# Optimization experiments

Measured on AMD Instinct MI355X. Metric: run time of the kernel, lower is better.

The kernel has to match this reference:

```python
import jax, jax.numpy as jnp
import numpy as np

N_NODES = 100000
N_EDGES = 600000
IN_SIZE = 128
OUT_SIZE = 128
N_GRAPHS = 100
BN_EPS = 1e-5


def setup_inputs() -> dict:
    key = jax.random.key(0)
    ks = jax.random.split(key, 8)
    h = jax.random.normal(ks[0], (N_NODES, IN_SIZE), dtype=jnp.float32)
    norm = jax.random.uniform(ks[1], (N_NODES, 1), dtype=jnp.float32)
    src = jax.random.randint(ks[2], (N_EDGES,), 0, N_NODES, dtype=jnp.int32)
    dst = jax.random.randint(ks[3], (N_EDGES,), 0, N_NODES, dtype=jnp.int32)
    graph_ids = jnp.sort(jax.random.randint(ks[4], (N_NODES,), 0, N_GRAPHS, dtype=jnp.int32))
    # Linear + BatchNorm params
    W = jax.random.normal(ks[5], (IN_SIZE, OUT_SIZE), dtype=jnp.float32) / np.sqrt(IN_SIZE)
    b = jnp.zeros((OUT_SIZE,), dtype=jnp.float32)
    gamma = jnp.ones((OUT_SIZE,), dtype=jnp.float32)
    beta = jnp.zeros((OUT_SIZE,), dtype=jnp.float32)
    return {"h": h, "norm": norm, "W": W, "b": b, "gamma": gamma, "beta": beta,
            "src": src, "dst": dst, "graph_ids": graph_ids}


def reference(h, norm, W, b, gamma, beta, src, dst, graph_ids):
    # pre-normalize, scatter-sum over edges (copy_src + sum), post-normalize
    x = h * norm                                            # [N, in]
    agg = jax.ops.segment_sum(x[src], dst, num_segments=N_NODES)  # SpMM
    x = agg * norm
    # linear + relu
    x = jax.nn.relu(jnp.dot(x, W) + b)                      # [N, out]
    # BatchNorm1d (training-mode: batch mean, biased variance)
    mean = jnp.mean(x, axis=0)
    var = jnp.mean(jnp.square(x - mean), axis=0)
    x = (x - mean) * jax.lax.rsqrt(var + BN_EPS) * gamma + beta
    # sum_nodes pooling per graph
    phis = jax.ops.segment_sum(x, graph_ids, num_segments=N_GRAPHS)  # [G, out]
    return (x, phis)
```

## Files before the change

kernel.cpp:

```cpp
#include <hip/hip_runtime.h>
#include <hip/hip_bf16.h>

#define N_NODES 100000
#define N_PAD 100096
#define N_EDGES 600000
#define CH 128
#define N_GRAPHS 100
#define BN_EPS 1e-5f
#define NBUCKET 32
#define CAP 16
#define OVFCAP 8192
#define EDGE_BLOCKS 2344
#define GEMM_BLOCKS 782
#define GATHER_BLOCKS 2048
#define BN_BLOCKS 1563
#define ZERO_INTS (N_NODES + 2 * NBUCKET * CH + 4)
#define ZERO_BLOCKS 423
#define PHIS_BLOCKS 50
#define WT_BLOCKS 64
#define PRESCALE_BLOCKS 6250

typedef __bf16 bf16x8 __attribute__((ext_vector_type(8)));
typedef float f32x4 __attribute__((ext_vector_type(4)));

__device__ __forceinline__ ushort f2bf(float f) {
    union { float f; unsigned u; } x; x.f = f;
    unsigned u = x.u;
    unsigned r = (u + 0x7fffu + ((u >> 16) & 1u)) >> 16;
    return (ushort)r;
}
__device__ __forceinline__ float bflo(unsigned p) { return __builtin_bit_cast(float, p << 16); }
__device__ __forceinline__ float bfhi(unsigned p) { return __builtin_bit_cast(float, p & 0xffff0000u); }

__global__ __launch_bounds__(256) void k_prep(const float* __restrict__ W,
        const float* __restrict__ h, const float* __restrict__ norm,
        int* __restrict__ zbase, ushort* __restrict__ Wt,
        float* __restrict__ phis, ushort* __restrict__ xh) {
    unsigned bid = blockIdx.x;
    int tid = threadIdx.x;
    if (bid < ZERO_BLOCKS) {
        int i = bid * 256 + tid;
        if (i < ZERO_INTS) zbase[i] = 0;
    } else if (bid < ZERO_BLOCKS + PHIS_BLOCKS) {
        int i = (bid - ZERO_BLOCKS) * 256 + tid;
        phis[i] = 0.f;
    } else if (bid < ZERO_BLOCKS + PHIS_BLOCKS + WT_BLOCKS) {
        int t = (bid - ZERO_BLOCKS - PHIS_BLOCKS) * 256 + tid;
        int k = t >> 7, o = t & 127;
        Wt[o * CH + k] = f2bf(W[t]);
    } else {
        int t = (bid - ZERO_BLOCKS - PHIS_BLOCKS - WT_BLOCKS) * 256 + tid;
        int n = t >> 4, c = (t & 15) << 3;
        float nm = norm[n];
        float4 a = *(const float4*)(h + (size_t)n * CH + c);
        float4 d = *(const float4*)(h + (size_t)n * CH + c + 4);
        uint4 o;
        o.x = (unsigned)f2bf(a.x * nm) | ((unsigned)f2bf(a.y * nm) << 16);
        o.y = (unsigned)f2bf(a.z * nm) | ((unsigned)f2bf(a.w * nm) << 16);
        o.z = (unsigned)f2bf(d.x * nm) | ((unsigned)f2bf(d.y * nm) << 16);
        o.w = (unsigned)f2bf(d.z * nm) | ((unsigned)f2bf(d.w * nm) << 16);
        *(uint4*)(xh + (size_t)n * CH + c) = o;
    }
}

__global__ __launch_bounds__(256) void k_fill(const int* __restrict__ src,
        const int* __restrict__ dst, int* __restrict__ cnt,
        int* __restrict__ ovfcur, int* __restrict__ ovf, int* __restrict__ esrc) {
    int e = blockIdx.x * 256 + threadIdx.x;
    if (e < N_EDGES) {
        int d = dst[e], s = src[e];
        int slot = atomicAdd(&cnt[d], 1);
        if (slot < CAP) __builtin_nontemporal_store(s, &esrc[d * CAP + slot]);
        else { int p = atomicAdd(ovfcur, 1); if (p < OVFCAP) { ovf[2*p] = d; ovf[2*p+1] = s; } }
    }
}

__global__ __launch_bounds__(256) void k_gather(const ushort* __restrict__ xh,
        const float* __restrict__ norm, const int* __restrict__ cnt,
        const int* __restrict__ esrc, const int* __restrict__ ovfcur,
        const int* __restrict__ ovf, ushort* __restrict__ x2) {
    int tid = threadIdx.x;
    int cg = tid & 15, rl = tid >> 4;
    int c = cg * 8;
    int no = min(*ovfcur, OVFCAP);

    for (int n = blockIdx.x * 16 + rl; n < N_PAD; n += GATHER_BLOCKS * 16) {
        if (n >= N_NODES) {
            uint4 z = {0u, 0u, 0u, 0u};
            *(uint4*)(x2 + (size_t)n * CH + c) = z;
            continue;
        }
        int craw = cnt[n];
        int e = min(craw, CAP);
        float nn = norm[n];
        int base = n * CAP;
        float a0=0.f,a1=0.f,a2=0.f,a3=0.f,a4=0.f,a5=0.f,a6=0.f,a7=0.f;
        int j = 0;
        for (; j + 4 <= e; j += 4) {
            int4 s4 = *(const int4*)(esrc + base + j);
            uint4 v0 = *(const uint4*)(xh + (size_t)s4.x * CH + c);
            uint4 v1 = *(const uint4*)(xh + (size_t)s4.y * CH + c);
            uint4 v2 = *(const uint4*)(xh + (size_t)s4.z * CH + c);
            uint4 v3 = *(const uint4*)(xh + (size_t)s4.w * CH + c);
            a0 += bflo(v0.x) + bflo(v1.x) + bflo(v2.x) + bflo(v3.x);
            a1 += bfhi(v0.x) + bfhi(v1.x) + bfhi(v2.x) + bfhi(v3.x);
            a2 += bflo(v0.y) + bflo(v1.y) + bflo(v2.y) + bflo(v3.y);
            a3 += bfhi(v0.y) + bfhi(v1.y) + bfhi(v2.y) + bfhi(v3.y);
            a4 += bflo(v0.z) + bflo(v1.z) + bflo(v2.z) + bflo(v3.z);
            a5 += bfhi(v0.z) + bfhi(v1.z) + bfhi(v2.z) + bfhi(v3.z);
            a6 += bflo(v0.w) + bflo(v1.w) + bflo(v2.w) + bflo(v3.w);
            a7 += bfhi(v0.w) + bfhi(v1.w) + bfhi(v2.w) + bfhi(v3.w);
        }
        for (; j < e; j++) {
            int s = esrc[base + j];
            uint4 v = *(const uint4*)(xh + (size_t)s * CH + c);
            a0 += bflo(v.x); a1 += bfhi(v.x);
            a2 += bflo(v.y); a3 += bfhi(v.y);
            a4 += bflo(v.z); a5 += bfhi(v.z);
            a6 += bflo(v.w); a7 += bfhi(v.w);
        }
        if (craw > CAP && no > 0) {
            for (int i = 0; i < no; i++) {
                if (ovf[2*i] == n) {
                    int s = ovf[2*i+1];
                    uint4 v = *(const uint4*)(xh + (size_t)s * CH + c);
                    a0 += bflo(v.x); a1 += bfhi(v.x);
                    a2 += bflo(v.y); a3 += bfhi(v.y);
                    a4 += bflo(v.z); a5 += bfhi(v.z);
                    a6 += bflo(v.w); a7 += bfhi(v.w);
                }
            }
        }
        uint4 o;
        o.x = (unsigned)f2bf(a0 * nn) | ((unsigned)f2bf(a1 * nn) << 16);
        o.y = (unsigned)f2bf(a2 * nn) | ((unsigned)f2bf(a3 * nn) << 16);
        o.z = (unsigned)f2bf(a4 * nn) | ((unsigned)f2bf(a5 * nn) << 16);
        o.w = (unsigned)f2bf(a6 * nn) | ((unsigned)f2bf(a7 * nn) << 16);
        *(uint4*)(x2 + (size_t)n * CH + c) = o;
    }
}

__global__ __launch_bounds__(256) void k_gemm(const ushort* __restrict__ x2,
        const ushort* __restrict__ Wt, const float* __restrict__ bias,
        ushort* __restrict__ y16, float* __restrict__ psum, float* __restrict__ psq) {
    __shared__ ushort ys[128 * CH];

    int tid = threadIdx.x;
    int w = tid >> 6, L = tid & 63;
    int c15 = L & 15, quad = L >> 4;
    size_t nb = (size_t)blockIdx.x * 128 + w * 32;

    const bf16x8* A0 = (const bf16x8*)(x2 + (nb + c15) * CH);
    const bf16x8* A1 = (const bf16x8*)(x2 + (nb + 16 + c15) * CH);

    f32x4 acc0[8] = {}, acc1[8] = {};
    #pragma unroll
    for (int kt = 0; kt < 4; kt++) {
        bf16x8 a0 = A0[kt * 4 + quad];
        bf16x8 a1 = A1[kt * 4 + quad];
        #pragma unroll
        for (int ot = 0; ot < 8; ot++) {
            bf16x8 b = *(const bf16x8*)(Wt + (size_t)(ot * 16 + c15) * CH + kt * 32 + quad * 8);
            acc0[ot] = __builtin_amdgcn_mfma_f32_16x16x32_bf16(a0, b, acc0[ot], 0, 0, 0);
            acc1[ot] = __builtin_amdgcn_mfma_f32_16x16x32_bf16(a1, b, acc1[ot], 0, 0, 0);
        }
    }

    float sA[8], qA[8];
    #pragma unroll
    for (int ot = 0; ot < 8; ot++) {
        int col = ot * 16 + c15;
        float bv = bias[col];
        float s_ = 0.f, q_ = 0.f;
        #pragma unroll
        for (int r = 0; r < 4; r++) {
            size_t n = nb + quad * 4 + r;
            float v = fmaxf(acc0[ot][r] + bv, 0.f);
            ys[(w * 32 + quad * 4 + r) * CH + col] = f2bf(v);
            if (n < N_NODES) { s_ += v; q_ += v * v; }
            size_t n2 = n + 16;
            float v2 = fmaxf(acc1[ot][r] + bv, 0.f);
            ys[(w * 32 + 16 + quad * 4 + r) * CH + col] = f2bf(v2);
            if (n2 < N_NODES) { s_ += v2; q_ += v2 * v2; }
        }
        sA[ot] = s_; qA[ot] = q_;
    }
    __syncthreads();

    {
        const uint4* ysv = (const uint4*)ys;
        uint4* out = (uint4*)(y16 + (size_t)blockIdx.x * 128 * CH);
        #pragma unroll
        for (int i = 0; i < 8; i++) out[tid + i * 256] = ysv[tid + i * 256];
    }
    __syncthreads();

    float* red = (float*)ys;
    #pragma unroll
    for (int ot = 0; ot < 8; ot++) {
        red[ot * 256 + tid] = sA[ot];
        red[2048 + ot * 256 + tid] = qA[ot];
    }
    __syncthreads();

    if (tid < 128) {
        int ot = tid >> 4, cc = tid & 15;
        int col = ot * 16 + cc;
        float S = 0.f, Q = 0.f;
        #pragma unroll
        for (int g = 0; g < 16; g++) {
            int sl = (g >> 2) * 64 + (g & 3) * 16 + cc;
            S += red[ot * 256 + sl];
            Q += red[2048 + ot * 256 + sl];
        }
        int bucket = blockIdx.x & (NBUCKET - 1);
        atomicAdd(&psum[bucket * CH + col], S);
        atomicAdd(&psq[bucket * CH + col], Q);
    }
}

__global__ void k_finalize(const float* __restrict__ psum, const float* __restrict__ psq,
        const float* __restrict__ gamma, const float* __restrict__ beta,
        float* __restrict__ scale, float* __restrict__ shift) {
    int t = threadIdx.x;
    float S = 0.f, Q = 0.f;
    #pragma unroll
    for (int g = 0; g < NBUCKET; g++) { S += psum[g * CH + t]; Q += psq[g * CH + t]; }
    const float invN = 1.f / (float)N_NODES;
    float mean = S * invN;
    float var  = Q * invN - mean * mean;
    float sc   = gamma[t] * rsqrtf(var + BN_EPS);
    scale[t] = sc;
    shift[t] = beta[t] - mean * sc;
}

__global__ __launch_bounds__(256) void k_bnpool(const ushort* __restrict__ y16,
        const int* __restrict__ gids, const float* __restrict__ scale,
        const float* __restrict__ shift, float* __restrict__ xout,
        float* __restrict__ phis) {
    __shared__ float smP[16][CH];

    int tid = threadIdx.x;
    int cg = tid & 15, rl = tid >> 4;
    int c = cg * 8;
    int r0 = blockIdx.x * 64;
    int rbase = r0 + rl * 4;

    float4 sc0 = *(const float4*)(scale + c), sc1 = *(const float4*)(scale + c + 4);
    float4 sh0 = *(const float4*)(shift + c), sh1 = *(const float4*)(shift + c + 4);

    bool fast = (r0 + 63 < N_NODES) && (gids[r0] == gids[r0 + 63]);

    if (fast) {
        float4 p0 = make_float4(0.f,0.f,0.f,0.f), p1 = make_float4(0.f,0.f,0.f,0.f);
        #pragma unroll
        for (int j = 0; j < 4; j++) {
            int r = rbase + j;
            uint4 v = *(const uint4*)(y16 + (size_t)r * CH + c);
            float4 f0, f1;
            f0.x = fmaf(bflo(v.x), sc0.x, sh0.x); f0.y = fmaf(bfhi(v.x), sc0.y, sh0.y);
            f0.z = fmaf(bflo(v.y), sc0.z, sh0.z); f0.w = fmaf(bfhi(v.y), sc0.w, sh0.w);
            f1.x = fmaf(bflo(v.z), sc1.x, sh1.x); f1.y = fmaf(bfhi(v.z), sc1.y, sh1.y);
            f1.z = fmaf(bflo(v.w), sc1.z, sh1.z); f1.w = fmaf(bfhi(v.w), sc1.w, sh1.w);
            *(float4*)(xout + (size_t)r * CH + c) = f0;
            *(float4*)(xout + (size_t)r * CH + c + 4) = f1;
            p0.x += f0.x; p0.y += f0.y; p0.z += f0.z; p0.w += f0.w;
            p1.x += f1.x; p1.y += f1.y; p1.z += f1.z; p1.w += f1.w;
        }
        *(float4*)&smP[rl][c] = p0;
        *(float4*)&smP[rl][c + 4] = p1;
        __syncthreads();
        if (tid < 128) {
            int g = gids[r0];
            float S = 0.f;
            #pragma unroll
            for (int k = 0; k < 16; k++) S += smP[k][tid];
            atomicAdd(&phis[(size_t)g * CH + tid], S);
        }
    } else {
        float p[8] = {};
        int gprev = -1;
        #pragma unroll
        for (int j = 0; j < 4; j++) {
            int r = rbase + j;
            if (r >= N_NODES) break;
            int g = gids[r];
            if (g != gprev) {
                if (gprev >= 0) {
                    #pragma unroll
                    for (int k = 0; k < 8; k++) {
                        atomicAdd(&phis[(size_t)gprev * CH + c + k], p[k]);
                        p[k] = 0.f;
                    }
                }
                gprev = g;
            }
            uint4 v = *(const uint4*)(y16 + (size_t)r * CH + c);
            float f[8];
            f[0] = fmaf(bflo(v.x), sc0.x, sh0.x); f[1] = fmaf(bfhi(v.x), sc0.y, sh0.y);
            f[2] = fmaf(bflo(v.y), sc0.z, sh0.z); f[3] = fmaf(bfhi(v.y), sc0.w, sh0.w);
            f[4] = fmaf(bflo(v.z), sc1.x, sh1.x); f[5] = fmaf(bfhi(v.z), sc1.y, sh1.y);
            f[6] = fmaf(bflo(v.w), sc1.z, sh1.z); f[7] = fmaf(bfhi(v.w), sc1.w, sh1.w);
            *(float4*)(xout + (size_t)r * CH + c) = make_float4(f[0], f[1], f[2], f[3]);
            *(float4*)(xout + (size_t)r * CH + c + 4) = make_float4(f[4], f[5], f[6], f[7]);
            #pragma unroll
            for (int k = 0; k < 8; k++) p[k] += f[k];
        }
        if (gprev >= 0) {
            #pragma unroll
            for (int k = 0; k < 8; k++)
                atomicAdd(&phis[(size_t)gprev * CH + c + k], p[k]);
        }
    }
}

extern "C" void kernel_launch(void* const* d_in, const int* in_sizes, int n_in,
                              void* d_out, int out_size, void* d_ws, size_t ws_size,
                              hipStream_t stream)
{
    const float* h     = (const float*)d_in[0];
    const float* norm  = (const float*)d_in[1];
    const float* W     = (const float*)d_in[2];
    const float* b     = (const float*)d_in[3];
    const float* gamma = (const float*)d_in[4];
    const float* beta  = (const float*)d_in[5];
    const int*   src   = (const int*)d_in[6];
    const int*   dst   = (const int*)d_in[7];
    const int*   gids  = (const int*)d_in[8];

    float* x_out = (float*)d_out;
    float* phis  = x_out + (size_t)N_NODES * CH;

    ushort* xh   = (ushort*)d_ws;
    ushort* x2   = xh + (size_t)N_NODES * CH;
    ushort* y16  = x2 + (size_t)N_PAD * CH;
    ushort* Wt   = y16 + (size_t)N_PAD * CH;
    int*   cnt     = (int*)(Wt + CH * CH);
    float* psum    = (float*)(cnt + N_NODES);
    float* psq     = psum + NBUCKET * CH;
    int*   ovfcur  = (int*)(psq + NBUCKET * CH);
    int*   esrc    = ovfcur + 4;
    int*   ovf     = esrc + (size_t)N_NODES * CAP;
    float* scale   = (float*)(ovf + 2 * OVFCAP);
    float* shift   = scale + CH;

    k_prep<<<ZERO_BLOCKS + PHIS_BLOCKS + WT_BLOCKS + PRESCALE_BLOCKS, 256, 0, stream>>>(
        W, h, norm, cnt, Wt, phis, xh);
    k_fill<<<EDGE_BLOCKS, 256, 0, stream>>>(src, dst, cnt, ovfcur, ovf, esrc);
    k_gather<<<GATHER_BLOCKS, 256, 0, stream>>>(
        xh, norm, cnt, esrc, ovfcur, ovf, x2);
    k_gemm<<<GEMM_BLOCKS, 256, 0, stream>>>(x2, Wt, b, y16, psum, psq);
    k_finalize<<<1, 128, 0, stream>>>(psum, psq, gamma, beta, scale, shift);
    k_bnpool<<<BN_BLOCKS, 256, 0, stream>>>(
        y16, gids, scale, shift, x_out, phis);
}
```

Baseline: 230.6 us.

## Fuse gather into GEMM via LDS, merge fill with prep, fold finalize into bnpool

The edge-fill pass is merged into the prep kernel, and the zeroing of counters and partial sums moves to a hipMemsetAsync. Gather and GEMM become one kernel that aggregates 128 rows into swizzled shared memory before running the MFMA tile, so the bf16 x2 intermediate is never written to or read from global memory. Each bnpool block now recomputes the BN scale and shift itself, which removes the single-block finalize launch. In exchange, the gather runs with only 782 blocks instead of 2048, which may expose less parallelism to hide the latency of random reads, and every bnpool block repeats the 32-bucket reduction.

```diff
diff --git a/kernel.cpp b/kernel.cpp
--- a/kernel.cpp
+++ b/kernel.cpp
@@ -10,15 +10,12 @@
 #define NBUCKET 32
 #define CAP 16
 #define OVFCAP 8192
-#define EDGE_BLOCKS 2344
-#define GEMM_BLOCKS 782
-#define GATHER_BLOCKS 2048
+#define FILL_BLOCKS 2344
+#define PRESCALE_BLOCKS 6250
+#define WT_BLOCKS 64
+#define PHIS_BLOCKS 50
+#define GG_BLOCKS 782
 #define BN_BLOCKS 1563
-#define ZERO_INTS (N_NODES + 2 * NBUCKET * CH + 4)
-#define ZERO_BLOCKS 423
-#define PHIS_BLOCKS 50
-#define WT_BLOCKS 64
-#define PRESCALE_BLOCKS 6250
 
 typedef __bf16 bf16x8 __attribute__((ext_vector_type(8)));
 typedef float f32x4 __attribute__((ext_vector_type(4)));
@@ -32,24 +29,24 @@
 __device__ __forceinline__ float bflo(unsigned p) { return __builtin_bit_cast(float, p << 16); }
 __device__ __forceinline__ float bfhi(unsigned p) { return __builtin_bit_cast(float, p & 0xffff0000u); }
 
-__global__ __launch_bounds__(256) void k_prep(const float* __restrict__ W,
-        const float* __restrict__ h, const float* __restrict__ norm,
-        int* __restrict__ zbase, ushort* __restrict__ Wt,
-        float* __restrict__ phis, ushort* __restrict__ xh) {
+__global__ __launch_bounds__(256) void k_front(const int* __restrict__ src,
+        const int* __restrict__ dst, const float* __restrict__ h,
+        const float* __restrict__ norm, const float* __restrict__ W,
+        int* __restrict__ cnt, int* __restrict__ ovfcur, int* __restrict__ ovf,
+        int* __restrict__ esrc, ushort* __restrict__ xh, ushort* __restrict__ Wt,
+        float* __restrict__ phis) {
     unsigned bid = blockIdx.x;
     int tid = threadIdx.x;
-    if (bid < ZERO_BLOCKS) {
-        int i = bid * 256 + tid;
-        if (i < ZERO_INTS) zbase[i] = 0;
-    } else if (bid < ZERO_BLOCKS + PHIS_BLOCKS) {
-        int i = (bid - ZERO_BLOCKS) * 256 + tid;
-        phis[i] = 0.f;
-    } else if (bid < ZERO_BLOCKS + PHIS_BLOCKS + WT_BLOCKS) {
-        int t = (bid - ZERO_BLOCKS - PHIS_BLOCKS) * 256 + tid;
-        int k = t >> 7, o = t & 127;
-        Wt[o * CH + k] = f2bf(W[t]);
-    } else {
-        int t = (bid - ZERO_BLOCKS - PHIS_BLOCKS - WT_BLOCKS) * 256 + tid;
+    if (bid < FILL_BLOCKS) {
+        int e = bid * 256 + tid;
+        if (e < N_EDGES) {
+            int d = dst[e], s = src[e];
+            int slot = atomicAdd(&cnt[d], 1);
+            if (slot < CAP) __builtin_nontemporal_store(s, &esrc[d * CAP + slot]);
+            else { int p = atomicAdd(ovfcur, 1); if (p < OVFCAP) { ovf[2*p] = d; ovf[2*p+1] = s; } }
+        }
+    } else if (bid < FILL_BLOCKS + PRESCALE_BLOCKS) {
+        int t = (bid - FILL_BLOCKS) * 256 + tid;
         int n = t >> 4, c = (t & 15) << 3;
         float nm = norm[n];
         float4 a = *(const float4*)(h + (size_t)n * CH + c);
@@ -60,74 +57,73 @@
         o.z = (unsigned)f2bf(d.x * nm) | ((unsigned)f2bf(d.y * nm) << 16);
         o.w = (unsigned)f2bf(d.z * nm) | ((unsigned)f2bf(d.w * nm) << 16);
         *(uint4*)(xh + (size_t)n * CH + c) = o;
-    }
-}
-
-__global__ __launch_bounds__(256) void k_fill(const int* __restrict__ src,
-        const int* __restrict__ dst, int* __restrict__ cnt,
-        int* __restrict__ ovfcur, int* __restrict__ ovf, int* __restrict__ esrc) {
-    int e = blockIdx.x * 256 + threadIdx.x;
-    if (e < N_EDGES) {
-        int d = dst[e], s = src[e];
-        int slot = atomicAdd(&cnt[d], 1);
-        if (slot < CAP) __builtin_nontemporal_store(s, &esrc[d * CAP + slot]);
-        else { int p = atomicAdd(ovfcur, 1); if (p < OVFCAP) { ovf[2*p] = d; ovf[2*p+1] = s; } }
-    }
-}
-
-__global__ __launch_bounds__(256) void k_gather(const ushort* __restrict__ xh,
+    } else if (bid < FILL_BLOCKS + PRESCALE_BLOCKS + WT_BLOCKS) {
+        int t = (bid - FILL_BLOCKS - PRESCALE_BLOCKS) * 256 + tid;
+        int k = t >> 7, o = t & 127;
+        Wt[o * CH + k] = f2bf(W[t]);
+    } else {
+        int i = (bid - FILL_BLOCKS - PRESCALE_BLOCKS - WT_BLOCKS) * 256 + tid;
+        phis[i] = 0.f;
+    }
+}
+
+__global__ __launch_bounds__(256) void k_gathergemm(const ushort* __restrict__ xh,
         const float* __restrict__ norm, const int* __restrict__ cnt,
         const int* __restrict__ esrc, const int* __restrict__ ovfcur,
-        const int* __restrict__ ovf, ushort* __restrict__ x2) {
+        const int* __restrict__ ovf, const float* __restrict__ bias,
+        const ushort* __restrict__ Wt, ushort* __restrict__ y16,
+        float* __restrict__ psum, float* __restrict__ psq) {
+    __shared__ ushort ys[128 * CH];
+
     int tid = threadIdx.x;
     int cg = tid & 15, rl = tid >> 4;
     int c = cg * 8;
     int no = min(*ovfcur, OVFCAP);
 
-    for (int n = blockIdx.x * 16 + rl; n < N_PAD; n += GATHER_BLOCKS * 16) {
-        if (n >= N_NODES) {
-            uint4 z = {0u, 0u, 0u, 0u};
-            *(uint4*)(x2 + (size_t)n * CH + c) = z;
-            continue;
-        }
-        int craw = cnt[n];
-        int e = min(craw, CAP);
-        float nn = norm[n];
-        int base = n * CAP;
+    for (int it = 0; it < 8; it++) {
+        int lr = it * 16 + rl;
+        int n = blockIdx.x * 128 + lr;
         float a0=0.f,a1=0.f,a2=0.f,a3=0.f,a4=0.f,a5=0.f,a6=0.f,a7=0.f;
-        int j = 0;
-        for (; j + 4 <= e; j += 4) {
-            int4 s4 = *(const int4*)(esrc + base + j);
-            uint4 v0 = *(const uint4*)(xh + (size_t)s4.x * CH + c);
-            uint4 v1 = *(const uint4*)(xh + (size_t)s4.y * CH + c);
-            uint4 v2 = *(const uint4*)(xh + (size_t)s4.z * CH + c);
-            uint4 v3 = *(const uint4*)(xh + (size_t)s4.w * CH + c);
-            a0 += bflo(v0.x) + bflo(v1.x) + bflo(v2.x) + bflo(v3.x);
-            a1 += bfhi(v0.x) + bfhi(v1.x) + bfhi(v2.x) + bfhi(v3.x);
-            a2 += bflo(v0.y) + bflo(v1.y) + bflo(v2.y) + bflo(v3.y);
-            a3 += bfhi(v0.y) + bfhi(v1.y) + bfhi(v2.y) + bfhi(v3.y);
-            a4 += bflo(v0.z) + bflo(v1.z) + bflo(v2.z) + bflo(v3.z);
-            a5 += bfhi(v0.z) + bfhi(v1.z) + bfhi(v2.z) + bfhi(v3.z);
-            a6 += bflo(v0.w) + bflo(v1.w) + bflo(v2.w) + bflo(v3.w);
-            a7 += bfhi(v0.w) + bfhi(v1.w) + bfhi(v2.w) + bfhi(v3.w);
-        }
-        for (; j < e; j++) {
-            int s = esrc[base + j];
-            uint4 v = *(const uint4*)(xh + (size_t)s * CH + c);
-            a0 += bflo(v.x); a1 += bfhi(v.x);
-            a2 += bflo(v.y); a3 += bfhi(v.y);
-            a4 += bflo(v.z); a5 += bfhi(v.z);
-            a6 += bflo(v.w); a7 += bfhi(v.w);
-        }
-        if (craw > CAP && no > 0) {
-            for (int i = 0; i < no; i++) {
-                if (ovf[2*i] == n) {
-                    int s = ovf[2*i+1];
-                    uint4 v = *(const uint4*)(xh + (size_t)s * CH + c);
-                    a0 += bflo(v.x); a1 += bfhi(v.x);
-                    a2 += bflo(v.y); a3 += bfhi(v.y);
-                    a4 += bflo(v.z); a5 += bfhi(v.z);
-                    a6 += bflo(v.w); a7 += bfhi(v.w);
+        float nn = 0.f;
+        if (n < N_NODES) {
+            int craw = cnt[n];
+            int e = min(craw, CAP);
+            nn = norm[n];
+            int base = n * CAP;
+            int j = 0;
+            for (; j + 4 <= e; j += 4) {
+                int4 s4 = *(const int4*)(esrc + base + j);
+                uint4 v0 = *(const uint4*)(xh + (size_t)s4.x * CH + c);
+                uint4 v1 = *(const uint4*)(xh + (size_t)s4.y * CH + c);
+                uint4 v2 = *(const uint4*)(xh + (size_t)s4.z * CH + c);
+                uint4 v3 = *(const uint4*)(xh + (size_t)s4.w * CH + c);
+                a0 += bflo(v0.x) + bflo(v1.x) + bflo(v2.x) + bflo(v3.x);
+                a1 += bfhi(v0.x) + bfhi(v1.x) + bfhi(v2.x) + bfhi(v3.x);
+                a2 += bflo(v0.y) + bflo(v1.y) + bflo(v2.y) + bflo(v3.y);
+                a3 += bfhi(v0.y) + bfhi(v1.y) + bfhi(v2.y) + bfhi(v3.y);
+                a4 += bflo(v0.z) + bflo(v1.z) + bflo(v2.z) + bflo(v3.z);
+                a5 += bfhi(v0.z) + bfhi(v1.z) + bfhi(v2.z) + bfhi(v3.z);
+                a6 += bflo(v0.w) + bflo(v1.w) + bflo(v2.w) + bflo(v3.w);
+                a7 += bfhi(v0.w) + bfhi(v1.w) + bfhi(v2.w) + bfhi(v3.w);
+            }
+            for (; j < e; j++) {
+                int s = esrc[base + j];
+                uint4 v = *(const uint4*)(xh + (size_t)s * CH + c);
+                a0 += bflo(v.x); a1 += bfhi(v.x);
+                a2 += bflo(v.y); a3 += bfhi(v.y);
+                a4 += bflo(v.z); a5 += bfhi(v.z);
+                a6 += bflo(v.w); a7 += bfhi(v.w);
+            }
+            if (craw > CAP && no > 0) {
+                for (int i = 0; i < no; i++) {
+                    if (ovf[2*i] == n) {
+                        int s = ovf[2*i+1];
+                        uint4 v = *(const uint4*)(xh + (size_t)s * CH + c);
+                        a0 += bflo(v.x); a1 += bfhi(v.x);
+                        a2 += bflo(v.y); a3 += bfhi(v.y);
+                        a4 += bflo(v.z); a5 += bfhi(v.z);
+                        a6 += bflo(v.w); a7 += bfhi(v.w);
+                    }
                 }
             }
         }
@@ -136,28 +132,21 @@
         o.y = (unsigned)f2bf(a2 * nn) | ((unsigned)f2bf(a3 * nn) << 16);
         o.z = (unsigned)f2bf(a4 * nn) | ((unsigned)f2bf(a5 * nn) << 16);
         o.w = (unsigned)f2bf(a6 * nn) | ((unsigned)f2bf(a7 * nn) << 16);
-        *(uint4*)(x2 + (size_t)n * CH + c) = o;
-    }
-}
-
-__global__ __launch_bounds__(256) void k_gemm(const ushort* __restrict__ x2,
-        const ushort* __restrict__ Wt, const float* __restrict__ bias,
-        ushort* __restrict__ y16, float* __restrict__ psum, float* __restrict__ psq) {
-    __shared__ ushort ys[128 * CH];
-
-    int tid = threadIdx.x;
+        *(uint4*)(ys + lr * CH + ((cg ^ (lr & 7)) << 3)) = o;
+    }
+    __syncthreads();
+
     int w = tid >> 6, L = tid & 63;
     int c15 = L & 15, quad = L >> 4;
+    int sw = c15 & 7;
     size_t nb = (size_t)blockIdx.x * 128 + w * 32;
-
-    const bf16x8* A0 = (const bf16x8*)(x2 + (nb + c15) * CH);
-    const bf16x8* A1 = (const bf16x8*)(x2 + (nb + 16 + c15) * CH);
 
     f32x4 acc0[8] = {}, acc1[8] = {};
     #pragma unroll
     for (int kt = 0; kt < 4; kt++) {
-        bf16x8 a0 = A0[kt * 4 + quad];
-        bf16x8 a1 = A1[kt * 4 + quad];
+        int chsw = ((kt * 4 + quad) ^ sw) << 3;
+        bf16x8 a0 = *(const bf16x8*)(ys + (w * 32 + c15) * CH + chsw);
+        bf16x8 a1 = *(const bf16x8*)(ys + (w * 32 + 16 + c15) * CH + chsw);
         #pragma unroll
         for (int ot = 0; ot < 8; ot++) {
             bf16x8 b = *(const bf16x8*)(Wt + (size_t)(ot * 16 + c15) * CH + kt * 32 + quad * 8);
@@ -165,6 +154,7 @@
             acc1[ot] = __builtin_amdgcn_mfma_f32_16x16x32_bf16(a1, b, acc1[ot], 0, 0, 0);
         }
     }
+    __syncthreads();
 
     float sA[8], qA[8];
     #pragma unroll
@@ -219,35 +209,35 @@
     }
 }
 
-__global__ void k_finalize(const float* __restrict__ psum, const float* __restrict__ psq,
-        const float* __restrict__ gamma, const float* __restrict__ beta,
-        float* __restrict__ scale, float* __restrict__ shift) {
-    int t = threadIdx.x;
-    float S = 0.f, Q = 0.f;
-    #pragma unroll
-    for (int g = 0; g < NBUCKET; g++) { S += psum[g * CH + t]; Q += psq[g * CH + t]; }
-    const float invN = 1.f / (float)N_NODES;
-    float mean = S * invN;
-    float var  = Q * invN - mean * mean;
-    float sc   = gamma[t] * rsqrtf(var + BN_EPS);
-    scale[t] = sc;
-    shift[t] = beta[t] - mean * sc;
-}
-
 __global__ __launch_bounds__(256) void k_bnpool(const ushort* __restrict__ y16,
-        const int* __restrict__ gids, const float* __restrict__ scale,
-        const float* __restrict__ shift, float* __restrict__ xout,
+        const int* __restrict__ gids, const float* __restrict__ psum,
+        const float* __restrict__ psq, const float* __restrict__ gamma,
+        const float* __restrict__ beta, float* __restrict__ xout,
         float* __restrict__ phis) {
     __shared__ float smP[16][CH];
+    __shared__ float ssc[CH], ssh[CH];
 
     int tid = threadIdx.x;
+    if (tid < 128) {
+        float S = 0.f, Q = 0.f;
+        #pragma unroll
+        for (int g = 0; g < NBUCKET; g++) { S += psum[g * CH + tid]; Q += psq[g * CH + tid]; }
+        const float invN = 1.f / (float)N_NODES;
+        float mean = S * invN;
+        float var  = Q * invN - mean * mean;
+        float sc   = gamma[tid] * rsqrtf(var + BN_EPS);
+        ssc[tid] = sc;
+        ssh[tid] = beta[tid] - mean * sc;
+    }
+    __syncthreads();
+
     int cg = tid & 15, rl = tid >> 4;
     int c = cg * 8;
     int r0 = blockIdx.x * 64;
     int rbase = r0 + rl * 4;
 
-    float4 sc0 = *(const float4*)(scale + c), sc1 = *(const float4*)(scale + c + 4);
-    float4 sh0 = *(const float4*)(shift + c), sh1 = *(const float4*)(shift + c + 4);
+    float4 sc0 = *(const float4*)&ssc[c], sc1 = *(const float4*)&ssc[c + 4];
+    float4 sh0 = *(const float4*)&ssh[c], sh1 = *(const float4*)&ssh[c + 4];
 
     bool fast = (r0 + 63 < N_NODES) && (gids[r0] == gids[r0 + 63]);
 
@@ -332,8 +322,7 @@
     float* phis  = x_out + (size_t)N_NODES * CH;
 
     ushort* xh   = (ushort*)d_ws;
-    ushort* x2   = xh + (size_t)N_NODES * CH;
-    ushort* y16  = x2 + (size_t)N_PAD * CH;
+    ushort* y16  = xh + (size_t)N_NODES * CH;
     ushort* Wt   = y16 + (size_t)N_PAD * CH;
     int*   cnt     = (int*)(Wt + CH * CH);
     float* psum    = (float*)(cnt + N_NODES);
@@ -341,16 +330,13 @@
     int*   ovfcur  = (int*)(psq + NBUCKET * CH);
     int*   esrc    = ovfcur + 4;
     int*   ovf     = esrc + (size_t)N_NODES * CAP;
-    float* scale   = (float*)(ovf + 2 * OVFCAP);
-    float* shift   = scale + CH;
-
-    k_prep<<<ZERO_BLOCKS + PHIS_BLOCKS + WT_BLOCKS + PRESCALE_BLOCKS, 256, 0, stream>>>(
-        W, h, norm, cnt, Wt, phis, xh);
-    k_fill<<<EDGE_BLOCKS, 256, 0, stream>>>(src, dst, cnt, ovfcur, ovf, esrc);
-    k_gather<<<GATHER_BLOCKS, 256, 0, stream>>>(
-        xh, norm, cnt, esrc, ovfcur, ovf, x2);
-    k_gemm<<<GEMM_BLOCKS, 256, 0, stream>>>(x2, Wt, b, y16, psum, psq);
-    k_finalize<<<1, 128, 0, stream>>>(psum, psq, gamma, beta, scale, shift);
+
+    hipMemsetAsync(cnt, 0, (size_t)(N_NODES + 2 * NBUCKET * CH + 4) * sizeof(int), stream);
+
+    k_front<<<FILL_BLOCKS + PRESCALE_BLOCKS + WT_BLOCKS + PHIS_BLOCKS, 256, 0, stream>>>(
+        src, dst, h, norm, W, cnt, ovfcur, ovf, esrc, xh, Wt, phis);
+    k_gathergemm<<<GG_BLOCKS, 256, 0, stream>>>(
+        xh, norm, cnt, esrc, ovfcur, ovf, b, Wt, y16, psum, psq);
     k_bnpool<<<BN_BLOCKS, 256, 0, stream>>>(
-        y16, gids, scale, shift, x_out, phis);
-}
+        y16, gids, psum, psq, gamma, beta, x_out, phis);
+}
```

Measured after the change: 251.0 us. 8.8% more time.
